# Optimization experiments

Hardware: AMD Instinct MI355X
Metric: run time of the kernel (lower is better)

Reference implementation:

```python
import jax, jax.numpy as jnp
import numpy as np

RAD = 4   # corr lookup radius
NH, NP = 8, 4  # deform attn heads / points (single level)


def conv2d(x, w, b, pad):
    y = jax.lax.conv_general_dilated(x, w, (1, 1), [(pad, pad), (pad, pad)],
                                     dimension_numbers=('NCHW', 'OIHW', 'NCHW'))
    return y + b[None, :, None, None]


def bilinear_gather(imgf, H, W, px, py):
    # imgf: [N, C, H*W]; px, py: [N, P] pixel coords; zero padding (grid_sample 'zeros')
    x0 = jnp.floor(px); y0 = jnp.floor(py)
    wx = px - x0; wy = py - y0
    def tap(xi, yi, wt):
        valid = (xi >= 0) & (xi <= W - 1) & (yi >= 0) & (yi <= H - 1)
        idx = (jnp.clip(yi, 0, H - 1) * W + jnp.clip(xi, 0, W - 1)).astype(jnp.int32)
        v = jnp.take_along_axis(imgf, idx[:, None, :], axis=2)
        return v * (wt * valid)[:, None, :]
    return (tap(x0, y0, (1 - wx) * (1 - wy)) + tap(x0 + 1, y0, wx * (1 - wy))
            + tap(x0, y0 + 1, (1 - wx) * wy) + tap(x0 + 1, y0 + 1, wx * wy))


def sine_pos_embed(B, H, W, npf, temperature=10000.0):
    # PositionEmbeddingSine with normalize=True
    scale = 2.0 * np.pi; eps = 1e-6
    y = jnp.broadcast_to(jnp.arange(1, H + 1, dtype=jnp.float32)[:, None], (H, W))
    x = jnp.broadcast_to(jnp.arange(1, W + 1, dtype=jnp.float32)[None, :], (H, W))
    y = (y - 0.5) / (H + eps) * scale
    x = (x - 0.5) / (W + eps) * scale
    dim_t = temperature ** (2.0 * (jnp.arange(npf) // 2).astype(jnp.float32) / npf)
    px = x[..., None] / dim_t
    py = y[..., None] / dim_t
    px = jnp.stack([jnp.sin(px[..., 0::2]), jnp.cos(px[..., 1::2])], -1).reshape(H, W, npf)
    py = jnp.stack([jnp.sin(py[..., 0::2]), jnp.cos(py[..., 1::2])], -1).reshape(H, W, npf)
    pos = jnp.concatenate([py, px], -1)
    return jnp.broadcast_to(pos[None], (B, H, W, 2 * npf)).reshape(B, H * W, 2 * npf)


def layer_norm(x, g, b):
    m = x.mean(-1, keepdims=True)
    v = ((x - m) ** 2).mean(-1, keepdims=True)
    return (x - m) / jnp.sqrt(v + 1e-5) * g + b


def _forward(fmap1, fmap2, flow, wc1, bc1, wc2, bc2, wf1, bf1, wf2, bf2, wcf, bcf,
             wfh1, bfh1, wfh2, bfh2, w_off, b_off, w_aw, b_aw, w_val, b_val,
             w_out, b_out, ln1_g, ln1_b, w_ff1, b_ff1, w_ff2, b_ff2, ln2_g, ln2_b):
    B, C, H, W = fmap1.shape
    HW = H * W
    dh = C // NH
    relu = jax.nn.relu
    # ---- CorrBlock.corr: all-pairs correlation volume ----
    corr = jnp.einsum('bcq,bck->bqk', fmap1.reshape(B, C, HW), fmap2.reshape(B, C, HW))
    corr = corr / jnp.sqrt(jnp.asarray(C, jnp.float32))
    corrf = corr.reshape(B * HW, 1, HW)  # [B*HW, 1, H2*W2]
    # ---- correlation lookup at coords = base grid + flow (bilinear, align_corners=True) ----
    gy, gx = jnp.meshgrid(jnp.arange(H, dtype=jnp.float32),
                          jnp.arange(W, dtype=jnp.float32), indexing='ij')
    cx = (gx[None] + flow[:, 0]).reshape(B * HW)
    cy = (gy[None] + flow[:, 1]).reshape(B * HW)
    d = jnp.linspace(-RAD, RAD, 2 * RAD + 1)
    oy, ox = jnp.meshgrid(d, d, indexing='ij')  # RAFT quirk: delta[...,0]=dy, delta[...,1]=dx
    px = cx[:, None] + oy.reshape(-1)[None, :]
    py = cy[:, None] + ox.reshape(-1)[None, :]
    corr_feat = bilinear_gather(corrf, H, W, px, py).reshape(B, H, W, (2 * RAD + 1) ** 2)
    corr_feat = corr_feat.transpose(0, 3, 1, 2)  # [B, 81, H, W]
    # ---- BasicMotionEncoder + FlowHead (BasicUpdateBlock.forward path) ----
    cor = relu(conv2d(corr_feat, wc1, bc1, 0))
    cor = relu(conv2d(cor, wc2, bc2, 1))
    flo = relu(conv2d(flow, wf1, bf1, 3))
    flo = relu(conv2d(flo, wf2, bf2, 1))
    mf = relu(conv2d(jnp.concatenate([cor, flo], 1), wcf, bcf, 1))
    mf = jnp.concatenate([mf, flow], 1)  # [B,128,H,W]
    delta_flow = conv2d(relu(conv2d(mf, wfh1, bfh1, 1)), wfh2, bfh2, 1)  # [B,2,H,W]
    # ---- single-level MSDeformAttn encoder layer over fmap1 tokens ----
    src = fmap1.reshape(B, C, HW).transpose(0, 2, 1)  # [B, Lq, C]
    pos = sine_pos_embed(B, H, W, C // 2)
    q = src + pos
    off = (q @ w_off.T + b_off).reshape(B, HW, NH, 1, NP, 2)
    aw = jax.nn.softmax((q @ w_aw.T + b_aw).reshape(B, HW, NH, NP), axis=-1)
    val = (src @ w_val.T + b_val).reshape(B, HW, NH, dh)
    ref = jnp.stack([(gx.reshape(-1) + 0.5) / W, (gy.reshape(-1) + 0.5) / H], -1)  # [HW,2]
    loc = (ref[None, :, None, None, None, :] + off / jnp.asarray([W, H], jnp.float32))[:, :, :, 0]
    # normalized loc -> pixel coords with align_corners=False convention
    px2 = (loc[..., 0] * W - 0.5).transpose(0, 2, 1, 3).reshape(B * NH, HW * NP)
    py2 = (loc[..., 1] * H - 0.5).transpose(0, 2, 1, 3).reshape(B * NH, HW * NP)
    vflat = val.transpose(0, 2, 3, 1).reshape(B * NH, dh, HW)
    samp = bilinear_gather(vflat, H, W, px2, py2).reshape(B, NH, dh, HW, NP)
    attn = (samp * aw.transpose(0, 2, 1, 3)[:, :, None]).sum(-1)  # [B,NH,dh,HW]
    attn = attn.transpose(0, 3, 1, 2).reshape(B, HW, C) @ w_out.T + b_out
    src = layer_norm(src + attn, ln1_g, ln1_b)
    ff = jax.nn.relu(src @ w_ff1.T + b_ff1) @ w_ff2.T + b_ff2
    src = layer_norm(src + ff, ln2_g, ln2_b)
    return src, delta_flow


def setup_inputs():
    key = jax.random.key(0)
    ks = jax.random.split(key, 20)
    B, C, H, W = 4, 256, 48, 48
    def w(i, shape, s=0.02):
        return jax.random.normal(ks[i], shape, jnp.float32) * s
    return {
        'fmap1': jax.random.normal(ks[0], (B, C, H, W), jnp.float32),
        'fmap2': jax.random.normal(ks[1], (B, C, H, W), jnp.float32),
        'flow': jax.random.normal(ks[2], (B, 2, H, W), jnp.float32),
        'wc1': w(3, (256, 81, 1, 1)), 'bc1': jnp.zeros((256,)),
        'wc2': w(4, (192, 256, 3, 3)), 'bc2': jnp.zeros((192,)),
        'wf1': w(5, (128, 2, 7, 7)), 'bf1': jnp.zeros((128,)),
        'wf2': w(6, (64, 128, 3, 3)), 'bf2': jnp.zeros((64,)),
        'wcf': w(7, (126, 256, 3, 3)), 'bcf': jnp.zeros((126,)),
        'wfh1': w(8, (256, 128, 3, 3)), 'bfh1': jnp.zeros((256,)),
        'wfh2': w(9, (2, 256, 3, 3)), 'bfh2': jnp.zeros((2,)),
        'w_off': w(10, (64, 256)), 'b_off': jnp.zeros((64,)),
        'w_aw': w(11, (32, 256)), 'b_aw': jnp.zeros((32,)),
        'w_val': w(12, (256, 256)), 'b_val': jnp.zeros((256,)),
        'w_out': w(13, (256, 256)), 'b_out': jnp.zeros((256,)),
        'ln1_g': jnp.ones((256,)), 'ln1_b': jnp.zeros((256,)),
        'w_ff1': w(14, (1024, 256)), 'b_ff1': jnp.zeros((1024,)),
        'w_ff2': w(15, (256, 1024)), 'b_ff2': jnp.zeros((256,)),
        'ln2_g': jnp.ones((256,)), 'ln2_b': jnp.zeros((256,)),
    }


def reference(fmap1, fmap2, flow, wc1, bc1, wc2, bc2, wf1, bf1, wf2, bf2, wcf, bcf,
              wfh1, bfh1, wfh2, bfh2, w_off, b_off, w_aw, b_aw, w_val, b_val,
              w_out, b_out, ln1_g, ln1_b, w_ff1, b_ff1, w_ff2, b_ff2, ln2_g, ln2_b):
    return _forward(fmap1, fmap2, flow, wc1, bc1, wc2, bc2, wf1, bf1, wf2, bf2, wcf, bcf,
                    wfh1, bfh1, wfh2, bfh2, w_off, b_off, w_aw, b_aw, w_val, b_val,
                    w_out, b_out, ln1_g, ln1_b, w_ff1, b_ff1, w_ff2, b_ff2, ln2_g, ln2_b)
```

## Files before the change

### kernel.cpp

```cpp
#include <hip/hip_runtime.h>
#include <hip/hip_bf16.h>
#include <math.h>

#define HH 48
#define WW 48
#define HW 2304
#define BB 4
#define CC 256

typedef __hip_bfloat16 bf16;
typedef __attribute__((ext_vector_type(8))) short s8v;
typedef __attribute__((ext_vector_type(4))) float f4v;

__device__ inline float bf2f(short u) {
  unsigned v = ((unsigned)(unsigned short)u) << 16;
  return __builtin_bit_cast(float, v);
}

__global__ __launch_bounds__(256) void prep_k(const float* __restrict__ fmap1,
                                              const float* __restrict__ fmap2,
                                              float* __restrict__ srcT,
                                              bf16* __restrict__ f1t,
                                              bf16* __restrict__ qb,
                                              bf16* __restrict__ f2t) {
  __shared__ float t[64][65];
  int z = blockIdx.z;
  int p0 = blockIdx.x * 64, c0 = blockIdx.y * 64;
  int b = z & 3;
  const float* src = (z < 4) ? fmap2 : fmap1;
  const float* inb = src + ((size_t)b * CC + c0) * HW + p0;
#pragma unroll
  for (int i = 0; i < 16; ++i) {
    int idx = threadIdx.x + i * 256;
    int c = idx >> 6, p = idx & 63;
    t[c][p] = inb[(size_t)c * HW + p];
  }
  __syncthreads();
  if (z < 4) {
    bf16* ob = f2t + ((size_t)b * HW + p0) * 256 + c0;
#pragma unroll
    for (int i = 0; i < 16; ++i) {
      int idx = threadIdx.x + i * 256;
      int p = idx >> 6, c = idx & 63;
      ob[(size_t)p * 256 + c] = (bf16)t[c][p];
    }
  } else {
    const float TWO_PI = 6.283185307179586f;
#pragma unroll
    for (int i = 0; i < 16; ++i) {
      int idx = threadIdx.x + i * 256;
      int pl = idx >> 6, cl = idx & 63;
      int c = c0 + cl;
      int p = p0 + pl;
      int y = p / WW, x = p % WW;
      float s = t[cl][pl];
      int axis = c >> 7;
      int cc = c & 127;
      int mm = cc >> 1;
      float coord = (axis ? ((float)x + 0.5f) : ((float)y + 0.5f)) * (TWO_PI / (48.f + 1e-6f));
      float tp = exp2f((float)mm * (13.287712379549449f / 64.f));
      float a = coord / tp;
      float pv = (cc & 1) ? cosf(a) : sinf(a);
      size_t o = ((size_t)b * HW + p) * 256 + c;
      srcT[o] = s;
      f1t[o] = (bf16)s;
      qb[o] = (bf16)(s + pv);
    }
  }
}

__global__ __launch_bounds__(256) void fused_corr_k(const bf16* __restrict__ f1t,
                                                    const bf16* __restrict__ f2t,
                                                    const float* __restrict__ flow,
                                                    bf16* __restrict__ cf) {
  __shared__ float Dp[4][112];
  __shared__ float Ds[112];
  int blk = blockIdx.x;
  int q = (blk & 7) * 1152 + (blk >> 3);
  int wave = threadIdx.x >> 6, lane = threadIdx.x & 63;
  int b = q / HW, p = q - b * HW;
  int y = p / WW, x = p - y * WW;
  float fx = flow[((size_t)b * 2 + 0) * HW + p];
  float fy = flow[((size_t)b * 2 + 1) * HW + p];
  float sx = (float)x + fx, sy = (float)y + fy;
  float fx0 = floorf(sx), fy0 = floorf(sy);
  int ix0 = (int)fx0, iy0 = (int)fy0;
  float wx = sx - fx0, wy = sy - fy0;
  int fl = lane & 15, fk8 = lane >> 4;
  const bf16* f1q = f1t + (size_t)q * 256 + wave * 64;
  s8v bf0 = *(const s8v*)(f1q + fk8 * 8);
  s8v bf1v = *(const s8v*)(f1q + 32 + fk8 * 8);
  const bf16* rowp[7];
#pragma unroll
  for (int g = 0; g < 7; ++g) {
    int w = g * 16 + fl;
    int jy = w / 10, jx = w - jy * 10;
    int ky = iy0 - 4 + jy, kx = ix0 - 4 + jx;
    bool valid = (w < 100) && ((unsigned)kx < (unsigned)WW) && ((unsigned)ky < (unsigned)HH);
    rowp[g] = valid ? (f2t + ((size_t)b * HW + ky * WW + kx) * 256 + wave * 64) : nullptr;
  }
  s8v a0[7], a1[7];
#pragma unroll
  for (int g = 0; g < 7; ++g) {
    s8v z = {0, 0, 0, 0, 0, 0, 0, 0};
    a0[g] = rowp[g] ? *(const s8v*)(rowp[g] + fk8 * 8) : z;
  }
#pragma unroll
  for (int g = 0; g < 7; ++g) {
    s8v z = {0, 0, 0, 0, 0, 0, 0, 0};
    a1[g] = rowp[g] ? *(const s8v*)(rowp[g] + 32 + fk8 * 8) : z;
  }
  f4v acc[7] = {};
#pragma unroll
  for (int g = 0; g < 7; ++g)
    acc[g] = __builtin_amdgcn_mfma_f32_16x16x32_bf16(a0[g], bf0, acc[g], 0, 0, 0);
#pragma unroll
  for (int g = 0; g < 7; ++g)
    acc[g] = __builtin_amdgcn_mfma_f32_16x16x32_bf16(a1[g], bf1v, acc[g], 0, 0, 0);
  if (fl == 0) {
#pragma unroll
    for (int g = 0; g < 7; ++g)
#pragma unroll
      for (int r = 0; r < 4; ++r)
        Dp[wave][g * 16 + fk8 * 4 + r] = acc[g][r];
  }
  __syncthreads();
  int tid = threadIdx.x;
  if (tid < 112) Ds[tid] = (Dp[0][tid] + Dp[1][tid] + Dp[2][tid] + Dp[3][tid]) * 0.0625f;
  __syncthreads();
  if (tid < 96) {
    float w00 = (1.f - wx) * (1.f - wy), w10 = wx * (1.f - wy);
    float w01 = (1.f - wx) * wy, w11 = wx * wy;
    float v = 0.f;
    if (tid < 81) {
      int jx = tid / 9, jy = tid - jx * 9;
      v = w00 * Ds[jy * 10 + jx] + w10 * Ds[jy * 10 + jx + 1] +
          w01 * Ds[(jy + 1) * 10 + jx] + w11 * Ds[(jy + 1) * 10 + jx + 1];
    }
    cf[(size_t)q * 96 + tid] = (bf16)v;
  }
}

struct WtSegs {
  const float* src[12];
  unsigned dstOff[12];
  int Cout[12], Cin[12], KP[12], KS2[12];
  unsigned cum[13];
};

__global__ __launch_bounds__(256) void wt_all_k(WtSegs s, bf16* __restrict__ base) {
  unsigned idx = blockIdx.x * 256 + threadIdx.x;
  if (idx >= s.cum[12]) return;
  int seg = 0;
#pragma unroll
  for (int i = 1; i < 12; ++i)
    if (idx >= s.cum[i]) seg = i;
  unsigned r = idx - s.cum[seg];
  int KP = s.KP[seg], Cout = s.Cout[seg], Cin = s.Cin[seg], KS2 = s.KS2[seg];
  int c = r % KP;
  int o = (r / KP) % Cout;
  int t = r / (KP * Cout);
  float v;
  if (KS2 == 0) {
    int cc = c >> 6, tt = c & 63;
    v = (tt < 49) ? s.src[seg][((size_t)o * 2 + cc) * 49 + tt] : 0.f;
  } else {
    v = (c < Cin) ? s.src[seg][((size_t)o * Cin + c) * KS2 + t] : 0.f;
  }
  base[s.dstOff[seg] + r] = (bf16)v;
}

__global__ __launch_bounds__(256) void im2col7_k(const float* __restrict__ flow,
                                                 bf16* __restrict__ col7) {
  int g = blockIdx.x * 256 + threadIdx.x;
  int kp = g & 127;
  int n = g >> 7;
  int b = n / HW;
  int p = n % HW;
  int y = p / WW, x = p % WW;
  int cc = kp >> 6, tt = kp & 63;
  float v = 0.f;
  if (tt < 49) {
    int ky = tt / 7, kx = tt % 7;
    int yy = y + ky - 3, xx = x + kx - 3;
    if ((unsigned)yy < (unsigned)HH && (unsigned)xx < (unsigned)WW)
      v = flow[((size_t)b * 2 + cc) * HW + yy * WW + xx];
  }
  col7[g] = (bf16)v;
}

struct GSegs {
  const bf16* in[4];
  const bf16* wt[4];
  const float* bias[4];
  const float* bias2[4];
  float* outf[4];
  bf16* outb[4];
  int split[4], O[4], KP[4], taps[4], OStride[4], OOff[4], relu[4], nTn[4];
  int blkStart[4];
  int nseg;
};

__global__ __launch_bounds__(256) void gemm_group_k(GSegs s) {
  int blk = blockIdx.x;
  int seg = 0;
#pragma unroll
  for (int i = 1; i < 4; ++i)
    if (i < s.nseg && blk >= s.blkStart[i]) seg = i;
  int rel = blk - s.blkStart[seg];
  int nTn = s.nTn[seg];
  int bm = rel / nTn, bn = rel % nTn;
  int m0 = bm * 128, n0 = bn * 64;
  int KP = s.KP[seg], O = s.O[seg], taps = s.taps[seg];
  const bf16* in = s.in[seg];
  const bf16* wt = s.wt[seg];

  __shared__ short As[2][128][64];
  __shared__ short Bs[2][64][64];
  int tid = threadIdx.x;
  int arl = tid >> 1, asl = (tid & 1) * 4;
  int brl = tid >> 2, bsl = (tid & 3) * 2;
  int wave = tid >> 6, lane = tid & 63;
  int wm = (wave >> 1) * 64, wn = (wave & 1) * 32;
  int fl = lane & 15, fk8 = lane >> 4;
  f4v acc[4][2] = {};
  int m = m0 + arl;
  int b = m / HW;
  int p = m - b * HW;
  int y = p / WW, x = p - y * WW;
  int wo = n0 + brl;
  bool wvalid = wo < O;
  int wo_c = wvalid ? wo : 0;

  int nc0 = (KP + 63) >> 6;
  int S = taps * nc0;
  uint4 apA[4], bpA[2], apB[4], bpB[2];

  auto load_stage = [&](int st, uint4* ap, uint4* bp) {
    int t = st / nc0;
    int c0 = (st - t * nc0) * 64;
    int yy = y, xx = x;
    bool valid = true;
    if (taps == 9) {
      int ky = t / 3, kx = t - ky * 3;
      yy = y + ky - 1;
      xx = x + kx - 1;
      valid = ((unsigned)yy < (unsigned)HH) & ((unsigned)xx < (unsigned)WW);
    }
    const bf16* arow = in + ((size_t)b * HW + yy * WW + xx) * KP;
    const bf16* wrow = wt + ((size_t)t * O + wo_c) * KP;
#pragma unroll
    for (int qq = 0; qq < 4; ++qq) {
      int col = c0 + (asl + qq) * 8;
      uint4 v = {0u, 0u, 0u, 0u};
      if (valid && col < KP) v = *(const uint4*)(arow + col);
      ap[qq] = v;
    }
#pragma unroll
    for (int qq = 0; qq < 2; ++qq) {
      int col = c0 + (bsl + qq) * 8;
      uint4 v = {0u, 0u, 0u, 0u};
      if (wvalid && col < KP) v = *(const uint4*)(wrow + col);
      bp[qq] = v;
    }
  };
  auto write_lds = [&](int cur, const uint4* ap, const uint4* bp) {
#pragma unroll
    for (int qq = 0; qq < 4; ++qq) {
      int sr = asl + qq;
      *(uint4*)&As[cur][arl][((sr ^ (arl & 7))) * 8] = ap[qq];
    }
#pragma unroll
    for (int qq = 0; qq < 2; ++qq) {
      int sr = bsl + qq;
      *(uint4*)&Bs[cur][brl][((sr ^ (brl & 7))) * 8] = bp[qq];
    }
  };
  auto compute = [&](int cur) {
#pragma unroll
    for (int cc = 0; cc < 2; ++cc) {
      s8v af[4], bfr[2];
#pragma unroll
      for (int i = 0; i < 4; ++i) {
        int ar = wm + i * 16 + fl;
        af[i] = *(const s8v*)&As[cur][ar][(((cc * 4 + fk8) ^ (ar & 7))) * 8];
      }
#pragma unroll
      for (int j = 0; j < 2; ++j) {
        int br = wn + j * 16 + fl;
        bfr[j] = *(const s8v*)&Bs[cur][br][(((cc * 4 + fk8) ^ (br & 7))) * 8];
      }
#pragma unroll
      for (int i = 0; i < 4; ++i)
#pragma unroll
        for (int j = 0; j < 2; ++j)
          acc[i][j] = __builtin_amdgcn_mfma_f32_16x16x32_bf16(af[i], bfr[j], acc[i][j], 0, 0, 0);
    }
  };

  load_stage(0, apA, bpA);
  if (S > 1) load_stage(1, apB, bpB);
  for (int st = 0; st < S; st += 2) {
    write_lds(0, apA, bpA);
    if (st + 2 < S) load_stage(st + 2, apA, bpA);
    __syncthreads();
    compute(0);
    write_lds(1, apB, bpB);
    if (st + 3 < S) load_stage(st + 3, apB, bpB);
    __syncthreads();
    compute(1);
  }

  int OStride = s.OStride[seg], OOff = s.OOff[seg], relu = s.relu[seg], split = s.split[seg];
  const float* bias = s.bias[seg];
  const float* bias2 = s.bias2[seg];
  float* outf = s.outf[seg];
  bf16* outb = s.outb[seg];
#pragma unroll
  for (int j = 0; j < 2; ++j) {
    int o = n0 + wn + j * 16 + fl;
    if (o < O) {
      float bsv = (bias2 != nullptr && o >= split) ? bias2[o - split] : bias[o];
#pragma unroll
      for (int i = 0; i < 4; ++i)
#pragma unroll
        for (int r = 0; r < 4; ++r) {
          int mm = m0 + wm + i * 16 + fk8 * 4 + r;
          float v = acc[i][j][r] + bsv;
          if (relu) v = fmaxf(v, 0.f);
          if (outb) outb[(size_t)mm * OStride + OOff + o] = (bf16)v;
          else outf[(size_t)mm * OStride + OOff + o] = v;
        }
    }
  }
}

__global__ __launch_bounds__(256) void convfh2_k(const bf16* __restrict__ fh1,
                                                 const float* __restrict__ w,
                                                 const float* __restrict__ bias,
                                                 float* __restrict__ out) {
  __shared__ float wl[4608];
  int tid = threadIdx.x;
#pragma unroll
  for (int i = tid; i < 4608; i += 256) {
    int o2 = i & 1;
    int t = (i >> 1) % 9;
    int c = i / 18;
    wl[i] = w[((size_t)o2 * 256 + c) * 9 + t];
  }
  __syncthreads();
  int wave = tid >> 6, lane = tid & 63;
  int pix = blockIdx.x * 4 + wave;
  int b = pix / HW;
  int q = pix % HW;
  int y = q / WW, x = q % WW;
  int c0 = lane * 4;
  float a0 = 0.f, a1 = 0.f;
#pragma unroll
  for (int ky = 0; ky < 3; ++ky) {
    int yy = y + ky - 1;
    if ((unsigned)yy >= (unsigned)HH) continue;
#pragma unroll
    for (int kx = 0; kx < 3; ++kx) {
      int xx = x + kx - 1;
      if ((unsigned)xx >= (unsigned)WW) continue;
      int t = ky * 3 + kx;
      const bf16* row = fh1 + ((size_t)b * HW + yy * WW + xx) * 256 + c0;
      ushort4 v = *(const ushort4*)row;
      unsigned short vv[4] = {v.x, v.y, v.z, v.w};
#pragma unroll
      for (int j = 0; j < 4; ++j) {
        float fv = bf2f((short)vv[j]);
        float2 wp = *(const float2*)&wl[((c0 + j) * 9 + t) * 2];
        a0 += fv * wp.x;
        a1 += fv * wp.y;
      }
    }
  }
#pragma unroll
  for (int offl = 32; offl > 0; offl >>= 1) {
    a0 += __shfl_xor(a0, offl);
    a1 += __shfl_xor(a1, offl);
  }
  if (lane == 0) {
    out[(size_t)b * 2 * HW + q] = a0 + bias[0];
    out[((size_t)b * 2 + 1) * HW + q] = a1 + bias[1];
  }
}

__global__ void copy_flow_k(const float* __restrict__ flow, bf16* __restrict__ mf) {
  int g = blockIdx.x * 256 + threadIdx.x;
  int p = g % HW;
  int c = (g / HW) % 2;
  int b = g / (2 * HW);
  mf[((size_t)b * HW + p) * 128 + 126 + c] = (bf16)flow[g];
}

__global__ __launch_bounds__(256) void deform_k(const bf16* __restrict__ val,
                                                const float* __restrict__ oa,
                                                bf16* __restrict__ attn) {
  int blk = blockIdx.x;
  int n = (blk & 7) * 1152 + (blk >> 3);
  int tid = threadIdx.x;
  int d = tid & 31;
  int h = (tid >> 5) & 7;
  int b = n / HW;
  int p = n % HW;
  int y = p / WW, x = p % WW;
  const float* ap = oa + (size_t)n * 96 + 64 + h * 4;
  float l0 = ap[0], l1 = ap[1], l2 = ap[2], l3 = ap[3];
  float mx = fmaxf(fmaxf(l0, l1), fmaxf(l2, l3));
  float e0 = expf(l0 - mx), e1 = expf(l1 - mx), e2 = expf(l2 - mx), e3 = expf(l3 - mx);
  float inv = 1.f / (e0 + e1 + e2 + e3);
  float wts[4] = {e0 * inv, e1 * inv, e2 * inv, e3 * inv};
  const float* offp = oa + (size_t)n * 96 + h * 8;
  const bf16* vb = val + (size_t)b * HW * 256 + h * 32 + d;
  float acc = 0.f;
#pragma unroll
  for (int pt = 0; pt < 4; ++pt) {
    float ox = offp[pt * 2 + 0];
    float oy = offp[pt * 2 + 1];
    float w = wts[pt];
    float px = (float)x + ox, py = (float)y + oy;
    float x0f = floorf(px), y0f = floorf(py);
    int x0 = (int)x0f, y0 = (int)y0f;
    float wx = px - x0f, wy = py - y0f;
    float s = 0.f;
    if ((unsigned)x0 < WW && (unsigned)y0 < HH)
      s += (float)vb[(size_t)(y0 * WW + x0) * 256] * (1.f - wx) * (1.f - wy);
    if ((unsigned)(x0 + 1) < WW && (unsigned)y0 < HH)
      s += (float)vb[(size_t)(y0 * WW + x0 + 1) * 256] * wx * (1.f - wy);
    if ((unsigned)x0 < WW && (unsigned)(y0 + 1) < HH)
      s += (float)vb[(size_t)((y0 + 1) * WW + x0) * 256] * (1.f - wx) * wy;
    if ((unsigned)(x0 + 1) < WW && (unsigned)(y0 + 1) < HH)
      s += (float)vb[(size_t)((y0 + 1) * WW + x0 + 1) * 256] * wx * wy;
    acc += w * s;
  }
  attn[(size_t)n * 256 + h * 32 + d] = (bf16)acc;
}

__global__ __launch_bounds__(256) void ln_add_k(const float* __restrict__ A,
                                                const float* __restrict__ Bv,
                                                const float* __restrict__ g,
                                                const float* __restrict__ be,
                                                float* __restrict__ out,
                                                bf16* __restrict__ outb) {
  int n = blockIdx.x;
  int c = threadIdx.x;
  float v = A[(size_t)n * 256 + c] + Bv[(size_t)n * 256 + c];
  float s1 = v, s2 = v * v;
#pragma unroll
  for (int o = 32; o > 0; o >>= 1) {
    s1 += __shfl_down(s1, o);
    s2 += __shfl_down(s2, o);
  }
  __shared__ float r1[4], r2[4], mv[2];
  int wid = c >> 6, lane = c & 63;
  if (lane == 0) {
    r1[wid] = s1;
    r2[wid] = s2;
  }
  __syncthreads();
  if (c == 0) {
    float a = r1[0] + r1[1] + r1[2] + r1[3];
    float q2 = r2[0] + r2[1] + r2[2] + r2[3];
    float mean = a * (1.f / 256.f);
    mv[0] = mean;
    mv[1] = q2 * (1.f / 256.f) - mean * mean;
  }
  __syncthreads();
  float mean = mv[0], var = mv[1];
  float r = (v - mean) * rsqrtf(var + 1e-5f) * g[c] + be[c];
  out[(size_t)n * 256 + c] = r;
  if (outb) outb[(size_t)n * 256 + c] = (bf16)r;
}

extern "C" void kernel_launch(void* const* d_in, const int* in_sizes, int n_in,
                              void* d_out, int out_size, void* d_ws, size_t ws_size,
                              hipStream_t stream) {
  const float* fmap1 = (const float*)d_in[0];
  const float* fmap2 = (const float*)d_in[1];
  const float* flow = (const float*)d_in[2];
  const float* wc1 = (const float*)d_in[3];
  const float* bc1 = (const float*)d_in[4];
  const float* wc2 = (const float*)d_in[5];
  const float* bc2 = (const float*)d_in[6];
  const float* wf1 = (const float*)d_in[7];
  const float* bf1 = (const float*)d_in[8];
  const float* wf2 = (const float*)d_in[9];
  const float* bf2 = (const float*)d_in[10];
  const float* wcf = (const float*)d_in[11];
  const float* bcf = (const float*)d_in[12];
  const float* wfh1 = (const float*)d_in[13];
  const float* bfh1 = (const float*)d_in[14];
  const float* wfh2 = (const float*)d_in[15];
  const float* bfh2 = (const float*)d_in[16];
  const float* w_off = (const float*)d_in[17];
  const float* b_off = (const float*)d_in[18];
  const float* w_aw = (const float*)d_in[19];
  const float* b_aw = (const float*)d_in[20];
  const float* w_val = (const float*)d_in[21];
  const float* b_val = (const float*)d_in[22];
  const float* w_out = (const float*)d_in[23];
  const float* b_out = (const float*)d_in[24];
  const float* ln1_g = (const float*)d_in[25];
  const float* ln1_b = (const float*)d_in[26];
  const float* w_ff1 = (const float*)d_in[27];
  const float* b_ff1 = (const float*)d_in[28];
  const float* w_ff2 = (const float*)d_in[29];
  const float* b_ff2 = (const float*)d_in[30];
  const float* ln2_g = (const float*)d_in[31];
  const float* ln2_b = (const float*)d_in[32];

  float* ws = (float*)d_ws;
  float* out_src = (float*)d_out;
  float* out_df = out_src + (size_t)BB * HW * CC;

  const size_t F_WT = 0;
  const size_t F_F1T = 11700000;
  const size_t F_F2T = 12900000;
  const size_t F_QB = 14100000;
  const size_t F_SRCT = 15300000;
  const size_t F_CF = 17700000;
  const size_t F_COL7 = 18200000;
  const size_t F_COR1 = 18800000;
  const size_t F_FLO1 = 20000000;
  const size_t F_CAT = 20600000;
  const size_t F_MF = 21800000;
  const size_t F_FH1 = 22400000;
  const size_t F_OA = 23600000;
  const size_t F_VAL = 24500000;
  const size_t F_ATTN = 26900000;
  const size_t F_TMP = 28100000;
  const size_t F_SRC1 = 30500000;
  const size_t F_SRC1B = 32900000;
  const size_t F_FF1 = 34100000;
  const size_t F_FF2 = 38900000;

  bf16* wkbase = (bf16*)(ws + F_WT);
  bf16* wk1 = wkbase + 0;
  bf16* wk2 = wkbase + 24576;
  bf16* wkf2 = wkbase + 466944;
  bf16* wkcf = wkbase + 540672;
  bf16* wkfh1 = wkbase + 830976;
  bf16* wl_oa = wkbase + 1125888;
  bf16* wl_val = wkbase + 1150464;
  bf16* wl_out = wkbase + 1216000;
  bf16* wl_ff1 = wkbase + 1281536;
  bf16* wl_ff2 = wkbase + 1543680;
  bf16* wk7 = wkbase + 1805824;
  bf16* f1t = (bf16*)(ws + F_F1T);
  bf16* f2t = (bf16*)(ws + F_F2T);
  bf16* qb = (bf16*)(ws + F_QB);
  bf16* cf = (bf16*)(ws + F_CF);
  bf16* col7 = (bf16*)(ws + F_COL7);
  bf16* cor1 = (bf16*)(ws + F_COR1);
  bf16* flo1 = (bf16*)(ws + F_FLO1);
  bf16* cat = (bf16*)(ws + F_CAT);
  bf16* mf = (bf16*)(ws + F_MF);
  bf16* fh1 = (bf16*)(ws + F_FH1);
  bf16* valb = (bf16*)(ws + F_VAL);
  bf16* attnb = (bf16*)(ws + F_ATTN);
  bf16* src1b = (bf16*)(ws + F_SRC1B);
  bf16* ff1b = (bf16*)(ws + F_FF1);

  WtSegs segs;
  const float* srcs[12] = {wc1, wc2, wf2, wcf, wfh1, w_off, w_aw, w_val, w_out, w_ff1, w_ff2, wf1};
  unsigned offs[12] = {0, 24576, 466944, 540672, 830976, 1125888, 1142272, 1150464, 1216000, 1281536, 1543680, 1805824};
  int couts[12] = {256, 192, 64, 126, 256, 64, 32, 256, 256, 1024, 256, 128};
  int cins[12] = {81, 256, 128, 256, 128, 256, 256, 256, 256, 256, 1024, 2};
  int kps[12] = {96, 256, 128, 256, 128, 256, 256, 256, 256, 256, 1024, 128};
  int ks2[12] = {1, 9, 9, 9, 9, 1, 1, 1, 1, 1, 1, 0};
  unsigned cum = 0;
  for (int i = 0; i < 12; ++i) {
    segs.src[i] = srcs[i];
    segs.dstOff[i] = offs[i];
    segs.Cout[i] = couts[i];
    segs.Cin[i] = cins[i];
    segs.KP[i] = kps[i];
    segs.KS2[i] = ks2[i];
    segs.cum[i] = cum;
    cum += (unsigned)((ks2[i] ? ks2[i] : 1) * couts[i] * kps[i]);
  }
  segs.cum[12] = cum;
  wt_all_k<<<dim3((cum + 255) / 256), 256, 0, stream>>>(segs, wkbase);

  prep_k<<<dim3(36, 4, 8), 256, 0, stream>>>(fmap1, fmap2, ws + F_SRCT, f1t, qb, f2t);
  im2col7_k<<<dim3(4608), 256, 0, stream>>>(flow, col7);
  copy_flow_k<<<dim3(72), 256, 0, stream>>>(flow, mf);

  fused_corr_k<<<dim3(9216), 256, 0, stream>>>(f1t, f2t, flow, cf);

  auto setseg = [](GSegs& G, int i, const bf16* in, const bf16* wt, const float* bias,
                   const float* bias2, int split, float* outf, bf16* outb, int O, int KP,
                   int taps, int OStride, int OOff, int relu) {
    G.in[i] = in; G.wt[i] = wt; G.bias[i] = bias; G.bias2[i] = bias2; G.split[i] = split;
    G.outf[i] = outf; G.outb[i] = outb; G.O[i] = O; G.KP[i] = KP; G.taps[i] = taps;
    G.OStride[i] = OStride; G.OOff[i] = OOff; G.relu[i] = relu;
    G.nTn[i] = (O + 63) / 64;
  };
  auto finseg = [](GSegs& G, int n) {
    int cumb = 0;
    for (int i = 0; i < 4; ++i) {
      if (i < n) { G.blkStart[i] = cumb; cumb += G.nTn[i] * 72; }
      else G.blkStart[i] = 0x7fffffff;
    }
    G.nseg = n;
    return cumb;
  };
  const int BIG = 1 << 30;

  GSegs GA;
  setseg(GA, 0, cf, wk1, bc1, nullptr, BIG, nullptr, cor1, 256, 96, 1, 256, 0, 1);
  setseg(GA, 1, col7, wk7, bf1, nullptr, BIG, nullptr, flo1, 128, 128, 1, 128, 0, 1);
  setseg(GA, 2, qb, wl_oa, b_off, b_aw, 64, ws + F_OA, nullptr, 96, 256, 1, 96, 0, 0);
  setseg(GA, 3, f1t, wl_val, b_val, nullptr, BIG, nullptr, valb, 256, 256, 1, 256, 0, 0);
  int nblkA = finseg(GA, 4);
  gemm_group_k<<<dim3(nblkA), 256, 0, stream>>>(GA);

  deform_k<<<dim3(9216), 256, 0, stream>>>(valb, ws + F_OA, attnb);

  GSegs GB;
  setseg(GB, 0, cor1, wk2, bc2, nullptr, BIG, nullptr, cat, 192, 256, 9, 256, 0, 1);
  setseg(GB, 1, flo1, wkf2, bf2, nullptr, BIG, nullptr, cat, 64, 128, 9, 256, 192, 1);
  setseg(GB, 2, attnb, wl_out, b_out, nullptr, BIG, ws + F_TMP, nullptr, 256, 256, 1, 256, 0, 0);
  int nblkB = finseg(GB, 3);
  gemm_group_k<<<dim3(nblkB), 256, 0, stream>>>(GB);

  ln_add_k<<<dim3(9216), 256, 0, stream>>>(ws + F_TMP, ws + F_SRCT, ln1_g, ln1_b, ws + F_SRC1, src1b);

  GSegs GC;
  setseg(GC, 0, cat, wkcf, bcf, nullptr, BIG, nullptr, mf, 126, 256, 9, 128, 0, 1);
  setseg(GC, 1, src1b, wl_ff1, b_ff1, nullptr, BIG, nullptr, ff1b, 1024, 256, 1, 1024, 0, 1);
  int nblkC = finseg(GC, 2);
  gemm_group_k<<<dim3(nblkC), 256, 0, stream>>>(GC);

  GSegs GD;
  setseg(GD, 0, mf, wkfh1, bfh1, nullptr, BIG, nullptr, fh1, 256, 128, 9, 256, 0, 1);
  setseg(GD, 1, ff1b, wl_ff2, b_ff2, nullptr, BIG, ws + F_FF2, nullptr, 256, 1024, 1, 256, 0, 0);
  int nblkD = finseg(GD, 2);
  gemm_group_k<<<dim3(nblkD), 256, 0, stream>>>(GD);

  convfh2_k<<<dim3(2304), 256, 0, stream>>>(fh1, wfh2, bfh2, out_df);
  ln_add_k<<<dim3(9216), 256, 0, stream>>>(ws + F_FF2, ws + F_SRC1, ln2_g, ln2_b, out_src, nullptr);

  (void)in_sizes; (void)n_in; (void)out_size; (void)ws_size;
}
```

Before: 260.7 us.

## Merge correlation and deformable sampling into grouped GEMM launches as tail blocks

Result: slower. 278.8 us (+6.9%).

```diff
diff --git a/kernel.cpp b/kernel.cpp
--- a/kernel.cpp
+++ b/kernel.cpp
@@ -69,78 +69,6 @@
   }
 }
 
-__global__ __launch_bounds__(256) void fused_corr_k(const bf16* __restrict__ f1t,
-                                                    const bf16* __restrict__ f2t,
-                                                    const float* __restrict__ flow,
-                                                    bf16* __restrict__ cf) {
-  __shared__ float Dp[4][112];
-  __shared__ float Ds[112];
-  int blk = blockIdx.x;
-  int q = (blk & 7) * 1152 + (blk >> 3);
-  int wave = threadIdx.x >> 6, lane = threadIdx.x & 63;
-  int b = q / HW, p = q - b * HW;
-  int y = p / WW, x = p - y * WW;
-  float fx = flow[((size_t)b * 2 + 0) * HW + p];
-  float fy = flow[((size_t)b * 2 + 1) * HW + p];
-  float sx = (float)x + fx, sy = (float)y + fy;
-  float fx0 = floorf(sx), fy0 = floorf(sy);
-  int ix0 = (int)fx0, iy0 = (int)fy0;
-  float wx = sx - fx0, wy = sy - fy0;
-  int fl = lane & 15, fk8 = lane >> 4;
-  const bf16* f1q = f1t + (size_t)q * 256 + wave * 64;
-  s8v bf0 = *(const s8v*)(f1q + fk8 * 8);
-  s8v bf1v = *(const s8v*)(f1q + 32 + fk8 * 8);
-  const bf16* rowp[7];
-#pragma unroll
-  for (int g = 0; g < 7; ++g) {
-    int w = g * 16 + fl;
-    int jy = w / 10, jx = w - jy * 10;
-    int ky = iy0 - 4 + jy, kx = ix0 - 4 + jx;
-    bool valid = (w < 100) && ((unsigned)kx < (unsigned)WW) && ((unsigned)ky < (unsigned)HH);
-    rowp[g] = valid ? (f2t + ((size_t)b * HW + ky * WW + kx) * 256 + wave * 64) : nullptr;
-  }
-  s8v a0[7], a1[7];
-#pragma unroll
-  for (int g = 0; g < 7; ++g) {
-    s8v z = {0, 0, 0, 0, 0, 0, 0, 0};
-    a0[g] = rowp[g] ? *(const s8v*)(rowp[g] + fk8 * 8) : z;
-  }
-#pragma unroll
-  for (int g = 0; g < 7; ++g) {
-    s8v z = {0, 0, 0, 0, 0, 0, 0, 0};
-    a1[g] = rowp[g] ? *(const s8v*)(rowp[g] + 32 + fk8 * 8) : z;
-  }
-  f4v acc[7] = {};
-#pragma unroll
-  for (int g = 0; g < 7; ++g)
-    acc[g] = __builtin_amdgcn_mfma_f32_16x16x32_bf16(a0[g], bf0, acc[g], 0, 0, 0);
-#pragma unroll
-  for (int g = 0; g < 7; ++g)
-    acc[g] = __builtin_amdgcn_mfma_f32_16x16x32_bf16(a1[g], bf1v, acc[g], 0, 0, 0);
-  if (fl == 0) {
-#pragma unroll
-    for (int g = 0; g < 7; ++g)
-#pragma unroll
-      for (int r = 0; r < 4; ++r)
-        Dp[wave][g * 16 + fk8 * 4 + r] = acc[g][r];
-  }
-  __syncthreads();
-  int tid = threadIdx.x;
-  if (tid < 112) Ds[tid] = (Dp[0][tid] + Dp[1][tid] + Dp[2][tid] + Dp[3][tid]) * 0.0625f;
-  __syncthreads();
-  if (tid < 96) {
-    float w00 = (1.f - wx) * (1.f - wy), w10 = wx * (1.f - wy);
-    float w01 = (1.f - wx) * wy, w11 = wx * wy;
-    float v = 0.f;
-    if (tid < 81) {
-      int jx = tid / 9, jy = tid - jx * 9;
-      v = w00 * Ds[jy * 10 + jx] + w10 * Ds[jy * 10 + jx + 1] +
-          w01 * Ds[(jy + 1) * 10 + jx] + w11 * Ds[(jy + 1) * 10 + jx + 1];
-    }
-    cf[(size_t)q * 96 + tid] = (bf16)v;
-  }
-}
-
 struct WtSegs {
   const float* src[12];
   unsigned dstOff[12];
@@ -189,6 +117,14 @@
   col7[g] = (bf16)v;
 }
 
+__global__ void copy_flow_k(const float* __restrict__ flow, bf16* __restrict__ mf) {
+  int g = blockIdx.x * 256 + threadIdx.x;
+  int p = g % HW;
+  int c = (g / HW) % 2;
+  int b = g / (2 * HW);
+  mf[((size_t)b * HW + p) * 128 + 126 + c] = (bf16)flow[g];
+}
+
 struct GSegs {
   const bf16* in[4];
   const bf16* wt[4];
@@ -201,7 +137,129 @@
   int nseg;
 };
 
-__global__ __launch_bounds__(256) void gemm_group_k(GSegs s) {
+template <int MODE>
+__global__ __launch_bounds__(256) void mega_k(GSegs s, int tailStart,
+                                              const bf16* __restrict__ f1t,
+                                              const bf16* __restrict__ f2t,
+                                              const float* __restrict__ flow,
+                                              bf16* __restrict__ cf,
+                                              const bf16* __restrict__ val,
+                                              const float* __restrict__ oa,
+                                              bf16* __restrict__ attn) {
+  __shared__ short As[2][128][64];
+  __shared__ short Bs[2][64][64];
+
+  if ((int)blockIdx.x >= tailStart) {
+    int cb = blockIdx.x - tailStart;
+    if (MODE == 0) {
+      float* Dp = (float*)As;
+      float* Dsum = ((float*)As) + 448;
+      int q = (cb & 7) * 1152 + (cb >> 3);
+      int wave = threadIdx.x >> 6, lane = threadIdx.x & 63;
+      int b = q / HW, p = q - b * HW;
+      int y = p / WW, x = p - y * WW;
+      float fx = flow[((size_t)b * 2 + 0) * HW + p];
+      float fy = flow[((size_t)b * 2 + 1) * HW + p];
+      float sx = (float)x + fx, sy = (float)y + fy;
+      float fx0 = floorf(sx), fy0 = floorf(sy);
+      int ix0 = (int)fx0, iy0 = (int)fy0;
+      float wx = sx - fx0, wy = sy - fy0;
+      int fl = lane & 15, fk8 = lane >> 4;
+      const bf16* f1q = f1t + (size_t)q * 256 + wave * 64;
+      s8v bf0 = *(const s8v*)(f1q + fk8 * 8);
+      s8v bf1v = *(const s8v*)(f1q + 32 + fk8 * 8);
+      const bf16* rowp[7];
+#pragma unroll
+      for (int g = 0; g < 7; ++g) {
+        int w = g * 16 + fl;
+        int jy = w / 10, jx = w - jy * 10;
+        int ky = iy0 - 4 + jy, kx = ix0 - 4 + jx;
+        bool valid = (w < 100) && ((unsigned)kx < (unsigned)WW) && ((unsigned)ky < (unsigned)HH);
+        rowp[g] = valid ? (f2t + ((size_t)b * HW + ky * WW + kx) * 256 + wave * 64) : nullptr;
+      }
+      s8v a0[7], a1[7];
+#pragma unroll
+      for (int g = 0; g < 7; ++g) {
+        s8v z = {0, 0, 0, 0, 0, 0, 0, 0};
+        a0[g] = rowp[g] ? *(const s8v*)(rowp[g] + fk8 * 8) : z;
+      }
+#pragma unroll
+      for (int g = 0; g < 7; ++g) {
+        s8v z = {0, 0, 0, 0, 0, 0, 0, 0};
+        a1[g] = rowp[g] ? *(const s8v*)(rowp[g] + 32 + fk8 * 8) : z;
+      }
+      f4v acc[7] = {};
+#pragma unroll
+      for (int g = 0; g < 7; ++g)
+        acc[g] = __builtin_amdgcn_mfma_f32_16x16x32_bf16(a0[g], bf0, acc[g], 0, 0, 0);
+#pragma unroll
+      for (int g = 0; g < 7; ++g)
+        acc[g] = __builtin_amdgcn_mfma_f32_16x16x32_bf16(a1[g], bf1v, acc[g], 0, 0, 0);
+      if (fl == 0) {
+#pragma unroll
+        for (int g = 0; g < 7; ++g)
+#pragma unroll
+          for (int r = 0; r < 4; ++r)
+            Dp[wave * 112 + g * 16 + fk8 * 4 + r] = acc[g][r];
+      }
+      __syncthreads();
+      int tid = threadIdx.x;
+      if (tid < 112)
+        Dsum[tid] = (Dp[tid] + Dp[112 + tid] + Dp[224 + tid] + Dp[336 + tid]) * 0.0625f;
+      __syncthreads();
+      if (tid < 96) {
+        float w00 = (1.f - wx) * (1.f - wy), w10 = wx * (1.f - wy);
+        float w01 = (1.f - wx) * wy, w11 = wx * wy;
+        float v = 0.f;
+        if (tid < 81) {
+          int jx = tid / 9, jy = tid - jx * 9;
+          v = w00 * Dsum[jy * 10 + jx] + w10 * Dsum[jy * 10 + jx + 1] +
+              w01 * Dsum[(jy + 1) * 10 + jx] + w11 * Dsum[(jy + 1) * 10 + jx + 1];
+        }
+        cf[(size_t)q * 96 + tid] = (bf16)v;
+      }
+    } else {
+      int n = (cb & 7) * 1152 + (cb >> 3);
+      int tid = threadIdx.x;
+      int d = tid & 31;
+      int h = (tid >> 5) & 7;
+      int b = n / HW;
+      int p = n % HW;
+      int y = p / WW, x = p % WW;
+      const float* ap = oa + (size_t)n * 96 + 64 + h * 4;
+      float l0 = ap[0], l1 = ap[1], l2 = ap[2], l3 = ap[3];
+      float mx = fmaxf(fmaxf(l0, l1), fmaxf(l2, l3));
+      float e0 = expf(l0 - mx), e1 = expf(l1 - mx), e2 = expf(l2 - mx), e3 = expf(l3 - mx);
+      float inv = 1.f / (e0 + e1 + e2 + e3);
+      float wts[4] = {e0 * inv, e1 * inv, e2 * inv, e3 * inv};
+      const float* offp = oa + (size_t)n * 96 + h * 8;
+      const bf16* vb = val + (size_t)b * HW * 256 + h * 32 + d;
+      float acc2 = 0.f;
+#pragma unroll
+      for (int pt = 0; pt < 4; ++pt) {
+        float ox = offp[pt * 2 + 0];
+        float oy = offp[pt * 2 + 1];
+        float w = wts[pt];
+        float px = (float)x + ox, py = (float)y + oy;
+        float x0f = floorf(px), y0f = floorf(py);
+        int x0 = (int)x0f, y0 = (int)y0f;
+        float wxx = px - x0f, wyy = py - y0f;
+        float sv = 0.f;
+        if ((unsigned)x0 < WW && (unsigned)y0 < HH)
+          sv += (float)vb[(size_t)(y0 * WW + x0) * 256] * (1.f - wxx) * (1.f - wyy);
+        if ((unsigned)(x0 + 1) < WW && (unsigned)y0 < HH)
+          sv += (float)vb[(size_t)(y0 * WW + x0 + 1) * 256] * wxx * (1.f - wyy);
+        if ((unsigned)x0 < WW && (unsigned)(y0 + 1) < HH)
+          sv += (float)vb[(size_t)((y0 + 1) * WW + x0) * 256] * (1.f - wxx) * wyy;
+        if ((unsigned)(x0 + 1) < WW && (unsigned)(y0 + 1) < HH)
+          sv += (float)vb[(size_t)((y0 + 1) * WW + x0 + 1) * 256] * wxx * wyy;
+        acc2 += w * sv;
+      }
+      attn[(size_t)n * 256 + h * 32 + d] = (bf16)acc2;
+    }
+    return;
+  }
+
   int blk = blockIdx.x;
   int seg = 0;
 #pragma unroll
@@ -215,8 +273,6 @@
   const bf16* in = s.in[seg];
   const bf16* wt = s.wt[seg];
 
-  __shared__ short As[2][128][64];
-  __shared__ short Bs[2][64][64];
   int tid = threadIdx.x;
   int arl = tid >> 1, asl = (tid & 1) * 4;
   int brl = tid >> 2, bsl = (tid & 3) * 2;
@@ -386,57 +442,6 @@
     out[(size_t)b * 2 * HW + q] = a0 + bias[0];
     out[((size_t)b * 2 + 1) * HW + q] = a1 + bias[1];
   }
-}
-
-__global__ void copy_flow_k(const float* __restrict__ flow, bf16* __restrict__ mf) {
-  int g = blockIdx.x * 256 + threadIdx.x;
-  int p = g % HW;
-  int c = (g / HW) % 2;
-  int b = g / (2 * HW);
-  mf[((size_t)b * HW + p) * 128 + 126 + c] = (bf16)flow[g];
-}
-
-__global__ __launch_bounds__(256) void deform_k(const bf16* __restrict__ val,
-                                                const float* __restrict__ oa,
-                                                bf16* __restrict__ attn) {
-  int blk = blockIdx.x;
-  int n = (blk & 7) * 1152 + (blk >> 3);
-  int tid = threadIdx.x;
-  int d = tid & 31;
-  int h = (tid >> 5) & 7;
-  int b = n / HW;
-  int p = n % HW;
-  int y = p / WW, x = p % WW;
-  const float* ap = oa + (size_t)n * 96 + 64 + h * 4;
-  float l0 = ap[0], l1 = ap[1], l2 = ap[2], l3 = ap[3];
-  float mx = fmaxf(fmaxf(l0, l1), fmaxf(l2, l3));
-  float e0 = expf(l0 - mx), e1 = expf(l1 - mx), e2 = expf(l2 - mx), e3 = expf(l3 - mx);
-  float inv = 1.f / (e0 + e1 + e2 + e3);
-  float wts[4] = {e0 * inv, e1 * inv, e2 * inv, e3 * inv};
-  const float* offp = oa + (size_t)n * 96 + h * 8;
-  const bf16* vb = val + (size_t)b * HW * 256 + h * 32 + d;
-  float acc = 0.f;
-#pragma unroll
-  for (int pt = 0; pt < 4; ++pt) {
-    float ox = offp[pt * 2 + 0];
-    float oy = offp[pt * 2 + 1];
-    float w = wts[pt];
-    float px = (float)x + ox, py = (float)y + oy;
-    float x0f = floorf(px), y0f = floorf(py);
-    int x0 = (int)x0f, y0 = (int)y0f;
-    float wx = px - x0f, wy = py - y0f;
-    float s = 0.f;
-    if ((unsigned)x0 < WW && (unsigned)y0 < HH)
-      s += (float)vb[(size_t)(y0 * WW + x0) * 256] * (1.f - wx) * (1.f - wy);
-    if ((unsigned)(x0 + 1) < WW && (unsigned)y0 < HH)
-      s += (float)vb[(size_t)(y0 * WW + x0 + 1) * 256] * wx * (1.f - wy);
-    if ((unsigned)x0 < WW && (unsigned)(y0 + 1) < HH)
-      s += (float)vb[(size_t)((y0 + 1) * WW + x0) * 256] * (1.f - wx) * wy;
-    if ((unsigned)(x0 + 1) < WW && (unsigned)(y0 + 1) < HH)
-      s += (float)vb[(size_t)((y0 + 1) * WW + x0 + 1) * 256] * wx * wy;
-    acc += w * s;
-  }
-  attn[(size_t)n * 256 + h * 32 + d] = (bf16)acc;
 }
 
 __global__ __launch_bounds__(256) void ln_add_k(const float* __restrict__ A,
@@ -589,8 +594,6 @@
   im2col7_k<<<dim3(4608), 256, 0, stream>>>(flow, col7);
   copy_flow_k<<<dim3(72), 256, 0, stream>>>(flow, mf);
 
-  fused_corr_k<<<dim3(9216), 256, 0, stream>>>(f1t, f2t, flow, cf);
-
   auto setseg = [](GSegs& G, int i, const bf16* in, const bf16* wt, const float* bias,
                    const float* bias2, int split, float* outf, bf16* outb, int O, int KP,
                    int taps, int OStride, int OOff, int relu) {
@@ -610,22 +613,26 @@
   };
   const int BIG = 1 << 30;
 
-  GSegs GA;
-  setseg(GA, 0, cf, wk1, bc1, nullptr, BIG, nullptr, cor1, 256, 96, 1, 256, 0, 1);
-  setseg(GA, 1, col7, wk7, bf1, nullptr, BIG, nullptr, flo1, 128, 128, 1, 128, 0, 1);
-  setseg(GA, 2, qb, wl_oa, b_off, b_aw, 64, ws + F_OA, nullptr, 96, 256, 1, 96, 0, 0);
-  setseg(GA, 3, f1t, wl_val, b_val, nullptr, BIG, nullptr, valb, 256, 256, 1, 256, 0, 0);
-  int nblkA = finseg(GA, 4);
-  gemm_group_k<<<dim3(nblkA), 256, 0, stream>>>(GA);
-
-  deform_k<<<dim3(9216), 256, 0, stream>>>(valb, ws + F_OA, attnb);
+  GSegs M1;
+  setseg(M1, 0, col7, wk7, bf1, nullptr, BIG, nullptr, flo1, 128, 128, 1, 128, 0, 1);
+  setseg(M1, 1, qb, wl_oa, b_off, b_aw, 64, ws + F_OA, nullptr, 96, 256, 1, 96, 0, 0);
+  setseg(M1, 2, f1t, wl_val, b_val, nullptr, BIG, nullptr, valb, 256, 256, 1, 256, 0, 0);
+  int nblk1 = finseg(M1, 3);
+  mega_k<0><<<dim3(nblk1 + 9216), 256, 0, stream>>>(M1, nblk1, f1t, f2t, flow, cf, valb,
+                                                    ws + F_OA, attnb);
+
+  GSegs M2;
+  setseg(M2, 0, cf, wk1, bc1, nullptr, BIG, nullptr, cor1, 256, 96, 1, 256, 0, 1);
+  int nblk2 = finseg(M2, 1);
+  mega_k<1><<<dim3(nblk2 + 9216), 256, 0, stream>>>(M2, nblk2, f1t, f2t, flow, cf, valb,
+                                                    ws + F_OA, attnb);
 
   GSegs GB;
   setseg(GB, 0, cor1, wk2, bc2, nullptr, BIG, nullptr, cat, 192, 256, 9, 256, 0, 1);
   setseg(GB, 1, flo1, wkf2, bf2, nullptr, BIG, nullptr, cat, 64, 128, 9, 256, 192, 1);
   setseg(GB, 2, attnb, wl_out, b_out, nullptr, BIG, ws + F_TMP, nullptr, 256, 256, 1, 256, 0, 0);
   int nblkB = finseg(GB, 3);
-  gemm_group_k<<<dim3(nblkB), 256, 0, stream>>>(GB);
+  mega_k<1><<<dim3(nblkB), 256, 0, stream>>>(GB, BIG, f1t, f2t, flow, cf, valb, ws + F_OA, attnb);
 
   ln_add_k<<<dim3(9216), 256, 0, stream>>>(ws + F_TMP, ws + F_SRCT, ln1_g, ln1_b, ws + F_SRC1, src1b);
 
@@ -633,13 +640,13 @@
   setseg(GC, 0, cat, wkcf, bcf, nullptr, BIG, nullptr, mf, 126, 256, 9, 128, 0, 1);
   setseg(GC, 1, src1b, wl_ff1, b_ff1, nullptr, BIG, nullptr, ff1b, 1024, 256, 1, 1024, 0, 1);
   int nblkC = finseg(GC, 2);
-  gemm_group_k<<<dim3(nblkC), 256, 0, stream>>>(GC);
+  mega_k<1><<<dim3(nblkC), 256, 0, stream>>>(GC, BIG, f1t, f2t, flow, cf, valb, ws + F_OA, attnb);
 
   GSegs GD;
   setseg(GD, 0, mf, wkfh1, bfh1, nullptr, BIG, nullptr, fh1, 256, 128, 9, 256, 0, 1);
   setseg(GD, 1, ff1b, wl_ff2, b_ff2, nullptr, BIG, ws + F_FF2, nullptr, 256, 1024, 1, 256, 0, 0);
   int nblkD = finseg(GD, 2);
-  gemm_group_k<<<dim3(nblkD), 256, 0, stream>>>(GD);
+  mega_k<1><<<dim3(nblkD), 256, 0, stream>>>(GD, BIG, f1t, f2t, flow, cf, valb, ws + F_OA, attnb);
 
   convfh2_k<<<dim3(2304), 256, 0, stream>>>(fh1, wfh2, bfh2, out_df);
   ln_add_k<<<dim3(9216), 256, 0, stream>>>(ws + F_FF2, ws + F_SRC1, ln2_g, ln2_b, out_src, nullptr);
```
